# Kernel tuning notes

Measured on AMD Instinct MI355X. Metric: run time of the kernel, lower is better.

The kernel has to match this reference:

```python
import jax, jax.numpy as jnp
import numpy as np

B, T, D = 4, 4096, 1024

def setup_inputs() -> dict:
    key = jax.random.key(0)
    ks = jax.random.split(key, 8)
    s = 1.0 / np.sqrt(D)
    return {
        "x": jax.random.normal(ks[0], (B, T, D), dtype=jnp.float32),
        # diagonal SSM params (per-channel)
        "A": jax.random.uniform(ks[1], (D,), dtype=jnp.float32, minval=0.5, maxval=0.99),  # stable decay
        "Bp": jax.random.normal(ks[2], (D,), dtype=jnp.float32) * 0.1,
        "Cp": jax.random.normal(ks[3], (D,), dtype=jnp.float32),
        # gate Linear
        "gate_w": jax.random.uniform(ks[4], (D, D), dtype=jnp.float32, minval=-s, maxval=s),
        "gate_b": jnp.zeros((D,), dtype=jnp.float32),
        # out Linear
        "out_w": jax.random.uniform(ks[5], (D, D), dtype=jnp.float32, minval=-s, maxval=s),
        "out_b": jnp.zeros((D,), dtype=jnp.float32),
    }

def _ssm(x, A, Bp, Cp):
    # diagonal linear recurrence: h_t = A*h_{t-1} + Bp*x_t ; y_t = Cp*h_t
    bx = x * Bp  # (B,T,D)
    def step(h, bx_t):
        h = A * h + bx_t  # (B,D)
        return h, h
    h0 = jnp.zeros((x.shape[0], x.shape[2]), dtype=x.dtype)
    _, hs = jax.lax.scan(step, h0, jnp.swapaxes(bx, 0, 1))  # (T,B,D)
    return jnp.swapaxes(hs, 0, 1) * Cp  # (B,T,D)

def reference(x, A, Bp, Cp, gate_w, gate_b, out_w, out_b):
    ssm_out = _ssm(x, A, Bp, Cp)
    gate = jax.nn.sigmoid(jnp.einsum('btd,ed->bte', x, gate_w) + gate_b)
    y = gate * ssm_out
    return jnp.einsum('btd,ed->bte', y, out_w) + out_b
```

## Files before the change

### kernel.cpp

```cpp
#include <hip/hip_runtime.h>
#include <hip/hip_bf16.h>
#include <cstdio>

typedef __hip_bfloat16 bf16;
typedef __bf16 bf16x8 __attribute__((ext_vector_type(8)));
typedef float f32x4 __attribute__((ext_vector_type(4)));

#define B_DIM 4
#define T_DIM 4096
#define D_DIM 1024
#define NC 64
#define LC 64

#define M_DIM (B_DIM * T_DIM)
#define BM 256
#define BN 256
#define BK 32
#define NT (D_DIM / BK)
#define GM (M_DIM / BM)
#define GN (D_DIM / BN)

static __device__ __forceinline__ float bfbits2f(unsigned short u) {
  return __uint_as_float(((unsigned)u) << 16);
}
static __device__ __forceinline__ unsigned short f2bfbits(float f) {
  bf16 v = __float2bfloat16(f);
  return *reinterpret_cast<unsigned short*>(&v);
}

__global__ __launch_bounds__(256) void cast_w_kernel(
    const float* __restrict__ gw, const float* __restrict__ ow,
    bf16* __restrict__ gw16, bf16* __restrict__ ow16, int n) {
  int i = blockIdx.x * 256 + threadIdx.x;
  if (i < n) {
    gw16[i] = __float2bfloat16(gw[i]);
    ow16[i] = __float2bfloat16(ow[i]);
  }
}

__global__ __launch_bounds__(256) void ssm_pass1(
    const float* __restrict__ x, const float* __restrict__ A,
    const float* __restrict__ Bp, float* __restrict__ hfin,
    unsigned short* __restrict__ x16) {
  const int tid  = threadIdx.x;
  const int half = blockIdx.x & 1;
  const int c    = (blockIdx.x >> 1) & (NC - 1);
  const int b    = blockIdx.x >> 7;
  const int d0   = half * 512 + tid * 2;
  const float a0 = A[d0], a1 = A[d0 + 1];
  const float bp0 = Bp[d0], bp1 = Bp[d0 + 1];
  const size_t base = (size_t)(b * T_DIM + c * LC) * D_DIM + d0;
  float h0 = 0.f, h1 = 0.f;
#pragma unroll 4
  for (int i = 0; i < LC; ++i) {
    const size_t o = base + (size_t)i * D_DIM;
    const float2 xv = *reinterpret_cast<const float2*>(x + o);
    const unsigned short u0 = f2bfbits(xv.x), u1 = f2bfbits(xv.y);
    const float f0 = bfbits2f(u0), f1 = bfbits2f(u1);
    h0 = fmaf(a0, h0, bp0 * f0);
    h1 = fmaf(a1, h1, bp1 * f1);
    *reinterpret_cast<ushort2*>(x16 + o) = make_ushort2(u0, u1);
  }
  const int ho = (b * NC + c) * D_DIM + d0;
  hfin[ho] = h0;
  hfin[ho + 1] = h1;
}

__global__ __launch_bounds__(256) void ssm_pass2(
    const float* __restrict__ A, const float* __restrict__ hfin,
    float* __restrict__ hin) {
  const int idx = blockIdx.x * 256 + threadIdx.x;
  const int d = idx & (D_DIM - 1);
  const int b = idx >> 10;
  float aL = A[d];
#pragma unroll
  for (int s = 0; s < 6; ++s) aL *= aL;
  float h = 0.f;
  for (int c = 0; c < NC; ++c) {
    const int o = (b * NC + c) * D_DIM + d;
    hin[o] = h;
    h = fmaf(aL, h, hfin[o]);
  }
}

template <bool GATE>
__global__ __launch_bounds__(512) void gemm256(
    const bf16* __restrict__ Xm, const bf16* __restrict__ Wm,
    const float* __restrict__ bias, const bf16* __restrict__ ssm,
    bf16* __restrict__ Ybf, float* __restrict__ Yf,
    const unsigned short* __restrict__ x16s, const float* __restrict__ Ap,
    const float* __restrict__ Bpp, const float* __restrict__ Cpp,
    const float* __restrict__ hinp) {
  __shared__ __align__(16) short LDS[4][16384];

  const int tid  = threadIdx.x;
  const int lane = tid & 63;
  const int wave = tid >> 6;
  const int wm = wave >> 2;
  const int wn = wave & 3;
  const int l15 = lane & 15;
  const int sA = ((lane >> 4) ^ ((l15 >> 1) & 3)) << 3;

  const int bid = blockIdx.x;
  const int swz = (bid & 7) * (GM * GN / 8) + (bid >> 3);
  const int m0 = (swz >> 2) * BM;
  const int n0 = (swz & 3) * BN;

  const int row0 = tid >> 2;
  const int c0   = (tid & 3) ^ ((row0 >> 1) & 3);
  const size_t offA0 = (size_t)(m0 + row0) * D_DIM + c0 * 8;
  const size_t offB0 = (size_t)(n0 + row0) * D_DIM + c0 * 8;

  auto gll = [](const bf16* g, short* l) {
    __builtin_amdgcn_global_load_lds(
        (const __attribute__((address_space(1))) void*)g,
        (__attribute__((address_space(3))) void*)l, 16, 0, 0);
  };
  auto STAGE = [&](int buf, int kt) {
    const size_t ko = (size_t)kt * BK;
    short* b0 = &LDS[buf][0] + wave * 512;
    gll(Xm + offA0 + ko,               b0);
    gll(Xm + offA0 + 128 * D_DIM + ko, b0 + 4096);
    gll(Wm + offB0 + ko,               b0 + 8192);
    gll(Wm + offB0 + 128 * D_DIM + ko, b0 + 12288);
  };

  f32x4 acc[8][4] = {};

  STAGE(0, 0);
  STAGE(1, 1);
  STAGE(2, 2);

  if (GATE) {
    unsigned short* ssms = (unsigned short*)ssm;
    const int bb_   = m0 >> 12;
    const int cbase = (m0 & 4095) >> 6;
#pragma unroll
    for (int p = 0; p < 2; ++p) {
      const int idx = p * 512 + tid;
      const int ch  = idx & 255;
      const int ck  = idx >> 8;
      const int d   = n0 + ch;
      const float a = Ap[d], bp = Bpp[d], cp = Cpp[d];
      float h = hinp[(bb_ * NC + cbase + ck) * D_DIM + d];
      size_t o = (size_t)(m0 + ck * 64) * D_DIM + d;
#pragma unroll 8
      for (int i = 0; i < LC; ++i, o += D_DIM) {
        h = fmaf(a, h, bp * bfbits2f(x16s[o]));
        ssms[o] = f2bfbits(cp * h);
      }
    }
  }

  asm volatile("s_waitcnt vmcnt(0)" ::: "memory");
  __builtin_amdgcn_s_barrier();

#define KTILE_BODY(T_, VMSTR, DO_STAGE, DO_BAR)                             \
  {                                                                         \
    const short* bb = &LDS[(T_) & 3][0];                                    \
    bf16x8 a[8], b[4];                                                      \
                      \
    _Pragma("unroll")                                                       \
    for (int i = 0; i < 4; ++i)                                             \
      a[i] = *(const bf16x8*)(bb + (wm * 128 + i * 16 + l15) * BK + sA);    \
    _Pragma("unroll")                                                       \
    for (int j = 0; j < 4; ++j)                                             \
      b[j] = *(const bf16x8*)(bb + 8192 + (wn * 64 + j * 16 + l15) * BK + sA); \
    _Pragma("unroll")                                                       \
    for (int i = 4; i < 8; ++i)                                             \
      a[i] = *(const bf16x8*)(bb + (wm * 128 + i * 16 + l15) * BK + sA);    \
    if (DO_STAGE) STAGE(((T_) + 3) & 3, (T_) + 3);                          \
    __builtin_amdgcn_s_setprio(1);                                          \
    _Pragma("unroll")                                                       \
    for (int i = 0; i < 4; ++i)                                             \
      _Pragma("unroll")                                                     \
      for (int j = 0; j < 4; ++j)                                           \
        acc[i][j] =                                                         \
            __builtin_amdgcn_mfma_f32_16x16x32_bf16(a[i], b[j], acc[i][j], 0, 0, 0); \
    __builtin_amdgcn_s_setprio(0);                                          \
    if (DO_BAR) {                                                           \
      asm volatile("s_waitcnt " VMSTR ::: "memory");                        \
      __builtin_amdgcn_s_barrier();                                         \
    }                                                                       \
    __builtin_amdgcn_s_setprio(1);                                          \
    _Pragma("unroll")                                                       \
    for (int i = 4; i < 8; ++i)                                             \
      _Pragma("unroll")                                                     \
      for (int j = 0; j < 4; ++j)                                           \
        acc[i][j] =                                                         \
            __builtin_amdgcn_mfma_f32_16x16x32_bf16(a[i], b[j], acc[i][j], 0, 0, 0); \
    __builtin_amdgcn_s_setprio(0);                                          \
  }

  for (int t = 0; t < NT - 3; ++t)
    KTILE_BODY(t, "vmcnt(8)", true, true);
  KTILE_BODY(NT - 3, "vmcnt(4)", false, true);
  KTILE_BODY(NT - 2, "vmcnt(0)", false, true);
  KTILE_BODY(NT - 1, "vmcnt(0)", false, false);
#undef KTILE_BODY

#pragma unroll
  for (int i = 0; i < 8; ++i) {
#pragma unroll
    for (int j = 0; j < 4; ++j) {
      const int col = n0 + wn * 64 + j * 16 + l15;
      const float bv = bias[col];
#pragma unroll
      for (int v = 0; v < 4; ++v) {
        const int row = m0 + wm * 128 + i * 16 + (lane >> 4) * 4 + v;
        const size_t o = (size_t)row * D_DIM + col;
        const float val = acc[i][j][v] + bv;
        if (GATE) {
          const float g = 1.f / (1.f + expf(-val));
          Ybf[o] = __float2bfloat16(g * __bfloat162float(ssm[o]));
        } else {
          Yf[o] = val;
        }
      }
    }
  }
}

extern "C" void kernel_launch(void* const* d_in, const int* in_sizes, int n_in,
                              void* d_out, int out_size, void* d_ws, size_t ws_size,
                              hipStream_t stream) {
  const float* x  = (const float*)d_in[0];
  const float* A  = (const float*)d_in[1];
  const float* Bp = (const float*)d_in[2];
  const float* Cp = (const float*)d_in[3];
  const float* gw = (const float*)d_in[4];
  const float* gb = (const float*)d_in[5];
  const float* ow = (const float*)d_in[6];
  const float* ob = (const float*)d_in[7];
  float* out = (float*)d_out;

  const size_t NEED = 73400320;
  if (ws_size < NEED) {
    fprintf(stderr, "kernel_launch: ws_size %zu < needed %zu\n", ws_size, NEED);
    return;
  }
  char* ws = (char*)d_ws;
  bf16*  x16   = (bf16*)(ws);
  bf16*  ssm16 = (bf16*)(ws + 33554432);
  bf16*  gw16  = (bf16*)(ws + 67108864);
  bf16*  ow16  = (bf16*)(ws + 69206016);
  float* hfin  = (float*)(ws + 71303168);
  float* hin   = (float*)(ws + 72351744);

  cast_w_kernel<<<(D_DIM * D_DIM) / 256, 256, 0, stream>>>(gw, ow, gw16, ow16, D_DIM * D_DIM);
  ssm_pass1<<<B_DIM * NC * 2, 256, 0, stream>>>(x, A, Bp, hfin,
                                                (unsigned short*)x16);
  ssm_pass2<<<(B_DIM * D_DIM) / 256, 256, 0, stream>>>(A, hfin, hin);

  gemm256<true><<<GM * GN, 512, 0, stream>>>(
      x16, gw16, gb, ssm16, ssm16, nullptr,
      (const unsigned short*)x16, A, Bp, Cp, hin);
  gemm256<false><<<GM * GN, 512, 0, stream>>>(
      ssm16, ow16, ob, nullptr, nullptr, out,
      nullptr, nullptr, nullptr, nullptr, nullptr);
}
```

Before: 126.7 us.

## Interleave SSM chunk recurrence with GEMM k-loop to overlap latency

The per-chunk SSM recurrence used to run serially before the GEMM main loop. It is now split into blocks of 4 timesteps, with each thread handling two chunks. Register double-buffered x loads are issued inside the first k-tiles of the gate GEMM, and the hand-tuned vmcnt counts are adjusted to cover the extra outstanding loads. The aim is to hide the recurrence's global-memory latency behind MFMA work, at the cost of more register pressure and fragile wait counts.

```diff
diff --git a/kernel.cpp b/kernel.cpp
--- a/kernel.cpp
+++ b/kernel.cpp
@@ -127,39 +127,53 @@
 
   f32x4 acc[8][4] = {};
 
+  float ar = 0.f, bpr = 0.f, cpr = 0.f, h0 = 0.f, h1 = 0.f;
+  size_t lo0 = 0, so0 = 0;
+  unsigned short* ssms = (unsigned short*)ssm;
+  unsigned short rlA[8], rlB[8];
+  if (GATE) {
+    const int ch = tid & 255;
+    const int ck = tid >> 8;
+    const int d  = n0 + ch;
+    ar = Ap[d]; bpr = Bpp[d]; cpr = Cpp[d];
+    const int bb_   = m0 >> 12;
+    const int cbase = (m0 & 4095) >> 6;
+    h0 = hinp[(bb_ * NC + cbase + ck) * D_DIM + d];
+    h1 = hinp[(bb_ * NC + cbase + ck + 2) * D_DIM + d];
+    lo0 = (size_t)(m0 + ck * 64) * D_DIM + d;
+    so0 = lo0;
+  }
+
   STAGE(0, 0);
   STAGE(1, 1);
   STAGE(2, 2);
-
-  if (GATE) {
-    unsigned short* ssms = (unsigned short*)ssm;
-    const int bb_   = m0 >> 12;
-    const int cbase = (m0 & 4095) >> 6;
-#pragma unroll
-    for (int p = 0; p < 2; ++p) {
-      const int idx = p * 512 + tid;
-      const int ch  = idx & 255;
-      const int ck  = idx >> 8;
-      const int d   = n0 + ch;
-      const float a = Ap[d], bp = Bpp[d], cp = Cpp[d];
-      float h = hinp[(bb_ * NC + cbase + ck) * D_DIM + d];
-      size_t o = (size_t)(m0 + ck * 64) * D_DIM + d;
-#pragma unroll 8
-      for (int i = 0; i < LC; ++i, o += D_DIM) {
-        h = fmaf(a, h, bp * bfbits2f(x16s[o]));
-        ssms[o] = f2bfbits(cp * h);
-      }
+  asm volatile("s_waitcnt vmcnt(8)" ::: "memory");
+  __builtin_amdgcn_s_barrier();
+
+#define RECBLK(RL_, MODE_)                                                  \
+    if (GATE && (MODE_) >= 2) {                                             \
+      _Pragma("unroll")                                                     \
+      for (int s = 0; s < 4; ++s) {                                         \
+        h0 = fmaf(ar, h0, bpr * bfbits2f(RL_[2 * s]));                      \
+        ssms[so0 + (size_t)s * D_DIM] = f2bfbits(cpr * h0);                 \
+        h1 = fmaf(ar, h1, bpr * bfbits2f(RL_[2 * s + 1]));                  \
+        ssms[so0 + (size_t)(128 + s) * D_DIM] = f2bfbits(cpr * h1);         \
+      }                                                                     \
+      so0 += 4 * D_DIM;                                                     \
+    }                                                                       \
+    if (GATE && ((MODE_) == 1 || (MODE_) == 2)) {                           \
+      _Pragma("unroll")                                                     \
+      for (int s = 0; s < 4; ++s) {                                         \
+        RL_[2 * s]     = x16s[lo0 + (size_t)s * D_DIM];                     \
+        RL_[2 * s + 1] = x16s[lo0 + (size_t)(128 + s) * D_DIM];             \
+      }                                                                     \
+      lo0 += 4 * D_DIM;                                                     \
     }
-  }
-
-  asm volatile("s_waitcnt vmcnt(0)" ::: "memory");
-  __builtin_amdgcn_s_barrier();
-
-#define KTILE_BODY(T_, VMSTR, DO_STAGE, DO_BAR)                             \
+
+#define KTILE_BODY(T_, VMSTR, DO_STAGE, DO_BAR, RL_, MODE_)                 \
   {                                                                         \
     const short* bb = &LDS[(T_) & 3][0];                                    \
     bf16x8 a[8], b[4];                                                      \
-                      \
     _Pragma("unroll")                                                       \
     for (int i = 0; i < 4; ++i)                                             \
       a[i] = *(const bf16x8*)(bb + (wm * 128 + i * 16 + l15) * BK + sA);    \
@@ -170,6 +184,7 @@
     for (int i = 4; i < 8; ++i)                                             \
       a[i] = *(const bf16x8*)(bb + (wm * 128 + i * 16 + l15) * BK + sA);    \
     if (DO_STAGE) STAGE(((T_) + 3) & 3, (T_) + 3);                          \
+    RECBLK(RL_, MODE_)                                                      \
     __builtin_amdgcn_s_setprio(1);                                          \
     _Pragma("unroll")                                                       \
     for (int i = 0; i < 4; ++i)                                             \
@@ -192,12 +207,30 @@
     __builtin_amdgcn_s_setprio(0);                                          \
   }
 
-  for (int t = 0; t < NT - 3; ++t)
-    KTILE_BODY(t, "vmcnt(8)", true, true);
-  KTILE_BODY(NT - 3, "vmcnt(4)", false, true);
-  KTILE_BODY(NT - 2, "vmcnt(0)", false, true);
-  KTILE_BODY(NT - 1, "vmcnt(0)", false, false);
+  if (GATE) {
+    KTILE_BODY(0, "vmcnt(16)", true, true, rlA, 1)
+    KTILE_BODY(1, "vmcnt(24)", true, true, rlB, 1)
+    KTILE_BODY(2, "vmcnt(40)", true, true, rlA, 2)
+    KTILE_BODY(3, "vmcnt(48)", true, true, rlB, 2)
+    for (int t = 4; t <= 14; t += 2) {
+      KTILE_BODY(t,     "vmcnt(56)", true, true, rlA, 2)
+      KTILE_BODY(t + 1, "vmcnt(56)", true, true, rlB, 2)
+    }
+    KTILE_BODY(16, "vmcnt(48)", true, true, rlA, 3)
+    KTILE_BODY(17, "vmcnt(40)", true, true, rlB, 3)
+    KTILE_BODY(18, "vmcnt(24)", true, true, rlA, 0)
+    KTILE_BODY(19, "vmcnt(16)", true, true, rlA, 0)
+    for (int t = 20; t < NT - 3; ++t)
+      KTILE_BODY(t, "vmcnt(8)", true, true, rlA, 0)
+  } else {
+    for (int t = 0; t < NT - 3; ++t)
+      KTILE_BODY(t, "vmcnt(8)", true, true, rlA, 0)
+  }
+  KTILE_BODY(NT - 3, "vmcnt(4)", false, true, rlA, 0)
+  KTILE_BODY(NT - 2, "vmcnt(0)", false, true, rlA, 0)
+  KTILE_BODY(NT - 1, "vmcnt(0)", false, false, rlA, 0)
 #undef KTILE_BODY
+#undef RECBLK
 
 #pragma unroll
   for (int i = 0; i < 8; ++i) {
```

New measurement: 125.4 us. About the same (-1.0%).

## Fold weight cast into SSM pass1 and inline chunk-prefix scan into gate GEMM

Applied to the files above, without the earlier changes.

Removes the separate weight-cast and ssm_pass2 kernels. The weight bf16 conversion now runs in 128 extra blocks of ssm_pass1, using vectorized float4 loads. Each gate-GEMM thread now rebuilds its chunk's starting state by scanning the earlier chunk final states (hfin) itself. This cuts two kernel launches and their serial dependencies, at the cost of redundant prefix work (up to 63 FMAs and loads per thread) in the GEMM prologue.

```diff
diff --git a/kernel.cpp b/kernel.cpp
--- a/kernel.cpp
+++ b/kernel.cpp
@@ -28,24 +28,31 @@
   return *reinterpret_cast<unsigned short*>(&v);
 }
 
-__global__ __launch_bounds__(256) void cast_w_kernel(
-    const float* __restrict__ gw, const float* __restrict__ ow,
-    bf16* __restrict__ gw16, bf16* __restrict__ ow16, int n) {
-  int i = blockIdx.x * 256 + threadIdx.x;
-  if (i < n) {
-    gw16[i] = __float2bfloat16(gw[i]);
-    ow16[i] = __float2bfloat16(ow[i]);
-  }
-}
-
 __global__ __launch_bounds__(256) void ssm_pass1(
     const float* __restrict__ x, const float* __restrict__ A,
     const float* __restrict__ Bp, float* __restrict__ hfin,
-    unsigned short* __restrict__ x16) {
+    unsigned short* __restrict__ x16,
+    const float* __restrict__ gw, const float* __restrict__ ow,
+    unsigned short* __restrict__ gw16, unsigned short* __restrict__ ow16) {
+  const int bidx = blockIdx.x;
+  if (bidx >= B_DIM * NC * 2) {
+    const int t = (bidx - B_DIM * NC * 2) * 256 + threadIdx.x;
+#pragma unroll
+    for (int j = 0; j < 8; ++j) {
+      const int e = t * 32 + j * 4;
+      const float4 g = *reinterpret_cast<const float4*>(gw + e);
+      const float4 o = *reinterpret_cast<const float4*>(ow + e);
+      *reinterpret_cast<ushort4*>(gw16 + e) = make_ushort4(
+          f2bfbits(g.x), f2bfbits(g.y), f2bfbits(g.z), f2bfbits(g.w));
+      *reinterpret_cast<ushort4*>(ow16 + e) = make_ushort4(
+          f2bfbits(o.x), f2bfbits(o.y), f2bfbits(o.z), f2bfbits(o.w));
+    }
+    return;
+  }
   const int tid  = threadIdx.x;
-  const int half = blockIdx.x & 1;
-  const int c    = (blockIdx.x >> 1) & (NC - 1);
-  const int b    = blockIdx.x >> 7;
+  const int half = bidx & 1;
+  const int c    = (bidx >> 1) & (NC - 1);
+  const int b    = bidx >> 7;
   const int d0   = half * 512 + tid * 2;
   const float a0 = A[d0], a1 = A[d0 + 1];
   const float bp0 = Bp[d0], bp1 = Bp[d0 + 1];
@@ -66,23 +73,6 @@
   hfin[ho + 1] = h1;
 }
 
-__global__ __launch_bounds__(256) void ssm_pass2(
-    const float* __restrict__ A, const float* __restrict__ hfin,
-    float* __restrict__ hin) {
-  const int idx = blockIdx.x * 256 + threadIdx.x;
-  const int d = idx & (D_DIM - 1);
-  const int b = idx >> 10;
-  float aL = A[d];
-#pragma unroll
-  for (int s = 0; s < 6; ++s) aL *= aL;
-  float h = 0.f;
-  for (int c = 0; c < NC; ++c) {
-    const int o = (b * NC + c) * D_DIM + d;
-    hin[o] = h;
-    h = fmaf(aL, h, hfin[o]);
-  }
-}
-
 template <bool GATE>
 __global__ __launch_bounds__(512) void gemm256(
     const bf16* __restrict__ Xm, const bf16* __restrict__ Wm,
@@ -90,7 +80,7 @@
     bf16* __restrict__ Ybf, float* __restrict__ Yf,
     const unsigned short* __restrict__ x16s, const float* __restrict__ Ap,
     const float* __restrict__ Bpp, const float* __restrict__ Cpp,
-    const float* __restrict__ hinp) {
+    const float* __restrict__ hfinp) {
   __shared__ __align__(16) short LDS[4][16384];
 
   const int tid  = threadIdx.x;
@@ -142,7 +132,13 @@
       const int ck  = idx >> 8;
       const int d   = n0 + ch;
       const float a = Ap[d], bp = Bpp[d], cp = Cpp[d];
-      float h = hinp[(bb_ * NC + cbase + ck) * D_DIM + d];
+      float aL = a;
+#pragma unroll
+      for (int s = 0; s < 6; ++s) aL *= aL;
+      float h = 0.f;
+      const int ce = cbase + ck;
+      for (int c = 0; c < ce; ++c)
+        h = fmaf(aL, h, hfinp[(bb_ * NC + c) * D_DIM + d]);
       size_t o = (size_t)(m0 + ck * 64) * D_DIM + d;
 #pragma unroll 8
       for (int i = 0; i < LC; ++i, o += D_DIM) {
@@ -159,7 +155,6 @@
   {                                                                         \
     const short* bb = &LDS[(T_) & 3][0];                                    \
     bf16x8 a[8], b[4];                                                      \
-                      \
     _Pragma("unroll")                                                       \
     for (int i = 0; i < 4; ++i)                                             \
       a[i] = *(const bf16x8*)(bb + (wm * 128 + i * 16 + l15) * BK + sA);    \
@@ -245,16 +240,14 @@
   bf16*  gw16  = (bf16*)(ws + 67108864);
   bf16*  ow16  = (bf16*)(ws + 69206016);
   float* hfin  = (float*)(ws + 71303168);
-  float* hin   = (float*)(ws + 72351744);
-
-  cast_w_kernel<<<(D_DIM * D_DIM) / 256, 256, 0, stream>>>(gw, ow, gw16, ow16, D_DIM * D_DIM);
-  ssm_pass1<<<B_DIM * NC * 2, 256, 0, stream>>>(x, A, Bp, hfin,
-                                                (unsigned short*)x16);
-  ssm_pass2<<<(B_DIM * D_DIM) / 256, 256, 0, stream>>>(A, hfin, hin);
+
+  ssm_pass1<<<B_DIM * NC * 2 + 128, 256, 0, stream>>>(
+      x, A, Bp, hfin, (unsigned short*)x16, gw, ow,
+      (unsigned short*)gw16, (unsigned short*)ow16);
 
   gemm256<true><<<GM * GN, 512, 0, stream>>>(
       x16, gw16, gb, ssm16, ssm16, nullptr,
-      (const unsigned short*)x16, A, Bp, Cp, hin);
+      (const unsigned short*)x16, A, Bp, Cp, hfin);
   gemm256<false><<<GM * GN, 512, 0, stream>>>(
       ssm16, ow16, ob, nullptr, nullptr, out,
       nullptr, nullptr, nullptr, nullptr, nullptr);
```

Result: slower. 134.4 us (+6.1%).
